# Kernel tuning notes

Hardware: AMD Instinct MI355X
Metric: run time of the kernel (lower is better)

Reference implementation:

```python
import jax, jax.numpy as jnp
import numpy as np

N = 65536      # total nodes
E = 655360     # total edges
G = 256        # graphs in batch
EGO = 64       # ego ids per graph (max(ego)+1)
S = G * EGO    # global ego segments
C_IN, H, P, OUT, L = 128, 128, 64, 10, 3
EPS = 1e-5


def setup_inputs() -> dict:
    key = jax.random.key(0)
    ks = jax.random.split(key, 8)
    x = jax.random.normal(ks[0], (N, C_IN), dtype=jnp.float32)
    edge_index = jax.random.randint(ks[1], (2, E), 0, N)
    batch = jnp.repeat(jnp.arange(G), N // G)          # sorted graph ids
    ego = jnp.arange(N) % EGO                           # every ego segment non-empty
    s = 1.0 / np.sqrt(H)
    w_root = jax.random.normal(ks[2], (L, H, H), jnp.float32) * s
    w_rel = jax.random.normal(ks[3], (L, H, H), jnp.float32) * s
    b_conv = jnp.zeros((L, H), jnp.float32)
    down_w = jax.random.normal(ks[4], (H, P), jnp.float32) * s
    w1 = jax.random.normal(ks[5], (P, 2 * OUT), jnp.float32) * (1.0 / np.sqrt(P))
    b1 = jnp.zeros((2 * OUT,), jnp.float32)
    gamma = jnp.ones((2 * OUT,), jnp.float32)
    beta = jnp.zeros((2 * OUT,), jnp.float32)
    w2 = jax.random.normal(ks[6], (2 * OUT, OUT), jnp.float32) * (1.0 / np.sqrt(2 * OUT))
    b2 = jnp.zeros((OUT,), jnp.float32)
    return dict(x=x, edge_index=edge_index, batch=batch, ego=ego,
                w_root=w_root, w_rel=w_rel, b_conv=b_conv, down_w=down_w,
                w1=w1, b1=b1, gamma=gamma, beta=beta, w2=w2, b2=b2)


def reference(x, edge_index, batch, ego, w_root, w_rel, b_conv, down_w,
              w1, b1, gamma, beta, w2, b2):
    src, dst = edge_index[0], edge_index[1]
    h = x
    for l in range(L):  # GraphConv: lin_rel(sum_{j->i} h_j) + lin_root(h_i) + b, then ReLU
        agg = jax.ops.segment_sum(h[src], dst, num_segments=N)      # [N,H]
        h = jax.nn.relu(agg @ w_rel[l] + h @ w_root[l] + b_conv[l])
    xi = h @ down_w                                                  # [N,P]
    ego_g = ego + batch * EGO                                        # global ego id
    pooled = jax.ops.segment_sum(xi, ego_g, num_segments=S)          # global_add_pool -> [S,P]
    seg_batch = jax.ops.segment_max(batch, ego_g, num_segments=S)    # global_max_pool(batch, ego) -> [S]
    # SoftmaxAggregation(t=1): per-feature softmax over ego segments within each graph
    m = jax.ops.segment_max(pooled, seg_batch, num_segments=G)       # [G,P]
    e = jnp.exp(pooled - m[seg_batch])
    denom = jax.ops.segment_sum(e, seg_batch, num_segments=G)
    alpha = jax.lax.stop_gradient(e / denom[seg_batch])              # semi_grad=True
    g = jax.ops.segment_sum(alpha * pooled, seg_batch, num_segments=G)  # [G,P]
    # PyG MLP([P, 2*OUT, OUT]): Linear -> BatchNorm (batch stats) -> ReLU -> Linear
    z = g @ w1 + b1
    mu = z.mean(axis=0)
    var = z.var(axis=0)
    z = (z - mu) / jnp.sqrt(var + EPS) * gamma + beta
    z = jax.nn.relu(z)
    return z @ w2 + b2                                               # [G,OUT]
```

## Files before the change

kernel.cpp:

```cpp
#include <hip/hip_runtime.h>
#include <hip/hip_bf16.h>

#define NN 65536
#define EE 655360
#define GG 256
#define EGOC 64
#define SS (GG*EGOC)
#define HH 128
#define PP 64
#define OUTD 10
#define LLAYERS 3
#define PADW 40
#define EPB1 5120
#define BCAP 4096

typedef __attribute__((ext_vector_type(8))) short short8_t;
typedef __attribute__((ext_vector_type(4))) float f32x4_t;

__device__ __forceinline__ unsigned short f2bf(float f){
  unsigned u = __float_as_uint(f);
  unsigned r = (u + 0x7fffu + ((u >> 16) & 1u)) >> 16;
  return (unsigned short)r;
}
__device__ __forceinline__ float bflo(unsigned v){ return __uint_as_float(v << 16); }
__device__ __forceinline__ float bfhi(unsigned v){ return __uint_as_float(v & 0xffff0000u); }

__global__ __launch_bounds__(256) void prep(const float* __restrict__ x,
    unsigned short* __restrict__ xb, int* __restrict__ bcur,
    const float* __restrict__ w_rel, const float* __restrict__ w_root,
    unsigned short* __restrict__ wt){
  const int b = blockIdx.x;
  if (b < 4096){
    if (b == 0) bcur[threadIdx.x] = 0;
    const size_t i = ((size_t)b * 256 + threadIdx.x) * 8;
    float4 a = *(const float4*)(x + i);
    float4 v = *(const float4*)(x + i + 4);
    uint4 o;
    o.x = f2bf(a.x) | ((unsigned)f2bf(a.y) << 16);
    o.y = f2bf(a.z) | ((unsigned)f2bf(a.w) << 16);
    o.z = f2bf(v.x) | ((unsigned)f2bf(v.y) << 16);
    o.w = f2bf(v.z) | ((unsigned)f2bf(v.w) << 16);
    *(uint4*)(xb + i) = o;
  } else {
    const int idx = (b - 4096) * 256 + threadIdx.x;
    const int mi = idx >> 14;
    const int n = (idx >> 7) & 127, k = idx & 127;
    const float* src = (mi & 1) ? w_root : w_rel;
    const int l = mi >> 1;
    wt[idx] = f2bf(src[(size_t)l * 16384 + (size_t)k * 128 + n]);
  }
}

__global__ __launch_bounds__(256) void bucket1(const int* __restrict__ src,
    const int* __restrict__ dst, int* __restrict__ bucket_cursor,
    unsigned* __restrict__ bdata){
  __shared__ int hist[256], lbase[256], cur[256], rbase[256];
  __shared__ unsigned staged[EPB1];
  const int t = threadIdx.x;
  const int e0 = blockIdx.x * EPB1;
  hist[t] = 0;
  __syncthreads();
  #pragma unroll
  for (int k = 0; k < EPB1/256; ++k){
    int d = dst[e0 + t + k*256];
    atomicAdd(&hist[d >> 8], 1);
  }
  __syncthreads();
  const int cnt = hist[t];
  int val = cnt;
  for (int off = 1; off < 256; off <<= 1){
    int y = (t >= off) ? hist[t - off] : 0;
    __syncthreads();
    val += y;
    hist[t] = val;
    __syncthreads();
  }
  const int excl = val - cnt;
  lbase[t] = excl;
  cur[t] = excl;
  rbase[t] = atomicAdd(&bucket_cursor[t], cnt);
  __syncthreads();
  #pragma unroll
  for (int k = 0; k < EPB1/256; ++k){
    int i = e0 + t + k*256;
    int d = dst[i];
    int s = src[i];
    int b = d >> 8;
    int p = atomicAdd(&cur[b], 1);
    staged[p] = (unsigned)s | ((unsigned)(d & 255) << 16) | ((unsigned)b << 24);
  }
  __syncthreads();
  #pragma unroll
  for (int k = 0; k < EPB1/256; ++k){
    int i = t + k*256;
    unsigned w = staged[i];
    int b = w >> 24;
    bdata[b * BCAP + rbase[b] + (i - lbase[b])] = w;
  }
}

__global__ __launch_bounds__(256) void bucket2(const unsigned* __restrict__ bdata,
    const int* __restrict__ bucket_cursor, int* __restrict__ rowptr,
    int* __restrict__ csr){
  __shared__ int hist[256], cur[256], red[256];
  const int t = threadIdx.x;
  const int b = blockIdx.x;
  red[t] = (t < b) ? bucket_cursor[t] : 0;
  hist[t] = 0;
  __syncthreads();
  for (int off = 128; off > 0; off >>= 1){
    if (t < off) red[t] += red[t + off];
    __syncthreads();
  }
  const int base = red[0];
  const int cnt = bucket_cursor[b];
  const unsigned* bd = bdata + (size_t)b * BCAP;
  for (int i = t; i < cnt; i += 256)
    atomicAdd(&hist[(bd[i] >> 16) & 255], 1);
  __syncthreads();
  const int c = hist[t];
  int val = c;
  for (int off = 1; off < 256; off <<= 1){
    int y = (t >= off) ? hist[t - off] : 0;
    __syncthreads();
    val += y;
    hist[t] = val;
    __syncthreads();
  }
  const int excl = val - c;
  cur[t] = excl;
  rowptr[(b << 8) + t] = base + excl;
  if (b == 255 && t == 255) rowptr[NN] = EE;
  __syncthreads();
  for (int i = t; i < cnt; i += 256){
    unsigned w = bd[i];
    int dl = (w >> 16) & 255;
    int p = atomicAdd(&cur[dl], 1);
    csr[base + p] = (int)(w & 0xFFFFu);
  }
}

__global__ __launch_bounds__(256) void agg_bf(const unsigned* __restrict__ hb,
    const int* __restrict__ rowptr, const int* __restrict__ csr,
    unsigned* __restrict__ aggb){
  const int wid = threadIdx.x >> 6;
  const int lane = threadIdx.x & 63;
  const int sub = lane >> 4;
  const int c = lane & 15;
  int node = (blockIdx.x << 2) + wid;

  int beg = rowptr[node];
  int end = rowptr[node + 1];
  int sw0, sw1, sw2, sw3;
  {
    int e0 = beg + sub, e1 = beg + 4 + sub, e2 = beg + 8 + sub, e3 = beg + 12 + sub;
    sw0 = csr[e0 < end ? e0 : beg];
    sw1 = csr[e1 < end ? e1 : beg];
    sw2 = csr[e2 < end ? e2 : beg];
    sw3 = csr[e3 < end ? e3 : beg];
  }

  for (int g = 0; g < 8; ++g){
    uint4 w0 = *(const uint4*)(hb + ((size_t)sw0 << 6) + (c << 2));
    uint4 w1 = *(const uint4*)(hb + ((size_t)sw1 << 6) + (c << 2));
    uint4 w2 = *(const uint4*)(hb + ((size_t)sw2 << 6) + (c << 2));
    uint4 w3 = *(const uint4*)(hb + ((size_t)sw3 << 6) + (c << 2));
    int nbeg = 0, nend = 0;
    if (g < 7){
      nbeg = rowptr[node + 8192];
      nend = rowptr[node + 8193];
    }
    float a0=0.f,a1=0.f,a2=0.f,a3=0.f,a4=0.f,a5=0.f,a6=0.f,a7=0.f;
    if (beg + sub      < end){ a0+=bflo(w0.x); a1+=bfhi(w0.x); a2+=bflo(w0.y); a3+=bfhi(w0.y);
                               a4+=bflo(w0.z); a5+=bfhi(w0.z); a6+=bflo(w0.w); a7+=bfhi(w0.w); }
    if (beg + 4 + sub  < end){ a0+=bflo(w1.x); a1+=bfhi(w1.x); a2+=bflo(w1.y); a3+=bfhi(w1.y);
                               a4+=bflo(w1.z); a5+=bfhi(w1.z); a6+=bflo(w1.w); a7+=bfhi(w1.w); }
    if (beg + 8 + sub  < end){ a0+=bflo(w2.x); a1+=bfhi(w2.x); a2+=bflo(w2.y); a3+=bfhi(w2.y);
                               a4+=bflo(w2.z); a5+=bfhi(w2.z); a6+=bflo(w2.w); a7+=bfhi(w2.w); }
    if (beg + 12 + sub < end){ a0+=bflo(w3.x); a1+=bfhi(w3.x); a2+=bflo(w3.y); a3+=bfhi(w3.y);
                               a4+=bflo(w3.z); a5+=bfhi(w3.z); a6+=bflo(w3.w); a7+=bfhi(w3.w); }
    for (int j = beg + 16; j < end; j += 16){
      #pragma unroll
      for (int u = 0; u < 4; ++u){
        const int e = j + (u << 2) + sub;
        if (e < end){
          const int s = csr[e];
          uint4 w = *(const uint4*)(hb + ((size_t)s << 6) + (c << 2));
          a0 += bflo(w.x); a1 += bfhi(w.x);
          a2 += bflo(w.y); a3 += bfhi(w.y);
          a4 += bflo(w.z); a5 += bfhi(w.z);
          a6 += bflo(w.w); a7 += bfhi(w.w);
        }
      }
    }
    a0 += __shfl_xor(a0, 16, 64); a1 += __shfl_xor(a1, 16, 64);
    a2 += __shfl_xor(a2, 16, 64); a3 += __shfl_xor(a3, 16, 64);
    a4 += __shfl_xor(a4, 16, 64); a5 += __shfl_xor(a5, 16, 64);
    a6 += __shfl_xor(a6, 16, 64); a7 += __shfl_xor(a7, 16, 64);
    a0 += __shfl_xor(a0, 32, 64); a1 += __shfl_xor(a1, 32, 64);
    a2 += __shfl_xor(a2, 32, 64); a3 += __shfl_xor(a3, 32, 64);
    a4 += __shfl_xor(a4, 32, 64); a5 += __shfl_xor(a5, 32, 64);
    a6 += __shfl_xor(a6, 32, 64); a7 += __shfl_xor(a7, 32, 64);
    if (lane < 16){
      uint4 o;
      o.x = (unsigned)f2bf(a0) | ((unsigned)f2bf(a1) << 16);
      o.y = (unsigned)f2bf(a2) | ((unsigned)f2bf(a3) << 16);
      o.z = (unsigned)f2bf(a4) | ((unsigned)f2bf(a5) << 16);
      o.w = (unsigned)f2bf(a6) | ((unsigned)f2bf(a7) << 16);
      *(uint4*)(aggb + ((size_t)node << 6) + (c << 2)) = o;
    }
    if (g < 7){
      node += 8192;
      beg = nbeg; end = nend;
      int e0 = beg + sub, e1 = beg + 4 + sub, e2 = beg + 8 + sub, e3 = beg + 12 + sub;
      sw0 = csr[e0 < end ? e0 : beg];
      sw1 = csr[e1 < end ? e1 : beg];
      sw2 = csr[e2 < end ? e2 : beg];
      sw3 = csr[e3 < end ? e3 : beg];
    }
  }
}

__global__ __launch_bounds__(256) void conv_mfma(
    const unsigned short* __restrict__ Aagg, const unsigned short* __restrict__ Ah,
    const unsigned short* __restrict__ wt,
    const float* __restrict__ bias,
    unsigned short* __restrict__ out){
  __shared__ unsigned short As[2][128 * PADW];
  __shared__ unsigned short Ws[2][128 * PADW];
  const int tid = threadIdx.x;
  const int row0 = blockIdx.x << 7;
  const int lane = tid & 63, wid = tid >> 6;
  const int wm64 = (wid >> 1) << 6;
  const int wn64 = (wid & 1) << 6;
  const int fr = lane & 15;
  const int fs = (lane >> 4) << 3;
  const int r0 = tid >> 2;
  const int s8 = (tid & 3) << 3;

  f32x4_t acc[4][4];
  #pragma unroll
  for (int i = 0; i < 4; ++i)
    #pragma unroll
    for (int j = 0; j < 4; ++j) acc[i][j] = (f32x4_t){0.f,0.f,0.f,0.f};

  uint4 ga0, ga1, gw0, gw1;

#define STAGE_LOAD(c) do{ \
    const unsigned short* Ap = ((c) < 4) ? Aagg : Ah; \
    const unsigned short* Wp = ((c) < 4) ? wt : (wt + 16384); \
    const int k0 = ((c) & 3) << 5; \
    ga0 = *(const uint4*)(Ap + (size_t)(row0 + r0) * 128 + k0 + s8); \
    ga1 = *(const uint4*)(Ap + (size_t)(row0 + 64 + r0) * 128 + k0 + s8); \
    gw0 = *(const uint4*)(Wp + (size_t)r0 * 128 + k0 + s8); \
    gw1 = *(const uint4*)(Wp + (size_t)(64 + r0) * 128 + k0 + s8); } while(0)
#define STAGE_WRITE(b) do{ \
    *(uint4*)&As[b][r0 * PADW + s8] = ga0; \
    *(uint4*)&As[b][(64 + r0) * PADW + s8] = ga1; \
    *(uint4*)&Ws[b][r0 * PADW + s8] = gw0; \
    *(uint4*)&Ws[b][(64 + r0) * PADW + s8] = gw1; } while(0)

  STAGE_LOAD(0);
  STAGE_WRITE(0);
  __syncthreads();

  for (int c = 0; c < 8; ++c){
    const int b = c & 1;
    if (c < 7) STAGE_LOAD(c + 1);

    short8_t af[4], wf[4];
    #pragma unroll
    for (int i = 0; i < 4; ++i)
      af[i] = *(const short8_t*)&As[b][(wm64 + i*16 + fr) * PADW + fs];
    #pragma unroll
    for (int j = 0; j < 4; ++j)
      wf[j] = *(const short8_t*)&Ws[b][(wn64 + j*16 + fr) * PADW + fs];
    #pragma unroll
    for (int j = 0; j < 4; ++j)
      #pragma unroll
      for (int i = 0; i < 4; ++i)
        acc[i][j] = __builtin_amdgcn_mfma_f32_16x16x32_bf16(wf[j], af[i], acc[i][j], 0, 0, 0);

    if (c < 7){
      STAGE_WRITE(b ^ 1);
      __syncthreads();
    }
  }
#undef STAGE_LOAD
#undef STAGE_WRITE

  #pragma unroll
  for (int j = 0; j < 4; ++j){
    const int n0 = wn64 + j*16 + ((lane >> 4) << 2);
    float4 b4 = *(const float4*)(bias + n0);
    #pragma unroll
    for (int i = 0; i < 4; ++i){
      const int m = row0 + wm64 + i*16 + fr;
      float v0 = fmaxf(acc[i][j][0] + b4.x, 0.f);
      float v1 = fmaxf(acc[i][j][1] + b4.y, 0.f);
      float v2 = fmaxf(acc[i][j][2] + b4.z, 0.f);
      float v3 = fmaxf(acc[i][j][3] + b4.w, 0.f);
      uint2 pk;
      pk.x = (unsigned)f2bf(v0) | ((unsigned)f2bf(v1) << 16);
      pk.y = (unsigned)f2bf(v2) | ((unsigned)f2bf(v3) << 16);
      *(uint2*)(out + (size_t)m * 128 + n0) = pk;
    }
  }
}

__global__ __launch_bounds__(256) void pool_soft(const unsigned* __restrict__ hb,
    const float* __restrict__ down_w, float* __restrict__ gout){
  __shared__ float wds[128 * 64];
  __shared__ float ps[64][64];
  __shared__ float hs[4][128];
  __shared__ float r1[4][64], r2[4][64];
  const int tid = threadIdx.x;
  const int g = blockIdx.x;
  for (int i = tid; i < 128 * 64 / 4; i += 256)
    ((float4*)wds)[i] = ((const float4*)down_w)[i];
  __syncthreads();
  const int wid = tid >> 6, lane = tid & 63;
  for (int it = 0; it < 16; ++it){
    const int e = (it << 2) + wid;
    const unsigned* hr = hb + (((size_t)(g * 256 + e)) << 6) + lane;
    float ax = 0.f, ay = 0.f;
    #pragma unroll
    for (int q = 0; q < 4; ++q){
      unsigned v = hr[(size_t)q * 64 * 64];
      ax += bflo(v); ay += bfhi(v);
    }
    hs[wid][(lane << 1) + 0] = ax;
    hs[wid][(lane << 1) + 1] = ay;
    float a0 = 0.f, a1 = 0.f, a2 = 0.f, a3 = 0.f;
    #pragma unroll
    for (int k = 0; k < 128; k += 4){
      a0 = fmaf(hs[wid][k + 0], wds[(k + 0) * 64 + lane], a0);
      a1 = fmaf(hs[wid][k + 1], wds[(k + 1) * 64 + lane], a1);
      a2 = fmaf(hs[wid][k + 2], wds[(k + 2) * 64 + lane], a2);
      a3 = fmaf(hs[wid][k + 3], wds[(k + 3) * 64 + lane], a3);
    }
    ps[e][lane] = (a0 + a1) + (a2 + a3);
  }
  __syncthreads();
  float m = -3.4e38f;
  #pragma unroll
  for (int r = 0; r < 16; ++r) m = fmaxf(m, ps[(wid << 4) + r][lane]);
  r1[wid][lane] = m;
  __syncthreads();
  m = fmaxf(fmaxf(r1[0][lane], r1[1][lane]), fmaxf(r1[2][lane], r1[3][lane]));
  __syncthreads();
  float se = 0.f, sn = 0.f;
  #pragma unroll
  for (int r = 0; r < 16; ++r){
    float p = ps[(wid << 4) + r][lane];
    float ev = expf(p - m);
    se += ev; sn += ev * p;
  }
  r1[wid][lane] = se; r2[wid][lane] = sn;
  __syncthreads();
  if (wid == 0){
    float d = (r1[0][lane] + r1[1][lane]) + (r1[2][lane] + r1[3][lane]);
    float n = (r2[0][lane] + r2[1][lane]) + (r2[2][lane] + r2[3][lane]);
    gout[(size_t)g * 64 + lane] = n / d;
  }
}

__global__ __launch_bounds__(256) void mlp_kernel(const float* __restrict__ gmat,
    const float* __restrict__ w1, const float* __restrict__ b1,
    const float* __restrict__ gamma, const float* __restrict__ beta,
    const float* __restrict__ w2, const float* __restrict__ b2,
    float* __restrict__ out){
  const int r = threadIdx.x;
  float z[20];
  #pragma unroll
  for (int j = 0; j < 20; ++j) z[j] = b1[j];
  for (int k = 0; k < 64; ++k){
    float gv = gmat[r*64 + k];
    #pragma unroll
    for (int j = 0; j < 20; ++j) z[j] = fmaf(gv, w1[k*20 + j], z[j]);
  }
  __shared__ float red1[4][20], red2[4][20];
  __shared__ float mu[20], istd[20];
  const int lane = r & 63, wid = r >> 6;
  #pragma unroll
  for (int j = 0; j < 20; ++j){
    float a = z[j], b = z[j]*z[j];
    #pragma unroll
    for (int off = 32; off > 0; off >>= 1){
      a += __shfl_xor(a, off, 64);
      b += __shfl_xor(b, off, 64);
    }
    if (lane == 0){ red1[wid][j] = a; red2[wid][j] = b; }
  }
  __syncthreads();
  if (r < 20){
    float m = red1[0][r] + red1[1][r] + red1[2][r] + red1[3][r];
    float q = red2[0][r] + red2[1][r] + red2[2][r] + red2[3][r];
    m *= (1.f/256.f); q *= (1.f/256.f);
    float var = q - m*m;
    mu[r] = m;
    istd[r] = 1.f / sqrtf(var + 1e-5f);
  }
  __syncthreads();
  float o[10];
  #pragma unroll
  for (int jo = 0; jo < 10; ++jo) o[jo] = b2[jo];
  #pragma unroll
  for (int j = 0; j < 20; ++j){
    float zn = (z[j] - mu[j]) * istd[j] * gamma[j] + beta[j];
    zn = fmaxf(zn, 0.f);
    #pragma unroll
    for (int jo = 0; jo < 10; ++jo) o[jo] = fmaf(zn, w2[j*10 + jo], o[jo]);
  }
  #pragma unroll
  for (int jo = 0; jo < 10; ++jo) out[r*10 + jo] = o[jo];
}

extern "C" void kernel_launch(void* const* d_in, const int* in_sizes, int n_in,
                              void* d_out, int out_size, void* d_ws, size_t ws_size,
                              hipStream_t stream){
  const float* x      = (const float*)d_in[0];
  const int*   eidx   = (const int*)d_in[1];
  const float* w_root = (const float*)d_in[4];
  const float* w_rel  = (const float*)d_in[5];
  const float* b_conv = (const float*)d_in[6];
  const float* down_w = (const float*)d_in[7];
  const float* w1     = (const float*)d_in[8];
  const float* b1     = (const float*)d_in[9];
  const float* gamma  = (const float*)d_in[10];
  const float* beta   = (const float*)d_in[11];
  const float* w2     = (const float*)d_in[12];
  const float* b2     = (const float*)d_in[13];
  const int* src = eidx;
  const int* dst = eidx + EE;

  char* wsp = (char*)d_ws;
  size_t off = 0;
  auto alloc = [&](size_t bytes)->char*{
    char* p = wsp + off;
    off += (bytes + 255) & ~(size_t)255;
    return p;
  };
  unsigned short* hb   = (unsigned short*)alloc((size_t)NN*HH*2);
  unsigned short* aggb = (unsigned short*)alloc((size_t)NN*HH*2);
  unsigned short* wtb  = (unsigned short*)alloc((size_t)6*128*128*2);
  int*      rowptr = (int*)     alloc((size_t)(NN+1)*4);
  int*      csr    = (int*)     alloc((size_t)EE*4);
  unsigned* bdata  = (unsigned*)alloc((size_t)256*BCAP*4);
  int*      bcur   = (int*)     alloc((size_t)256*4);
  float*    gout   = (float*)   alloc((size_t)GG*PP*4);

  prep<<<4096 + 384, 256, 0, stream>>>(x, hb, bcur, w_rel, w_root, wtb);
  bucket1<<<EE/EPB1, 256, 0, stream>>>(src, dst, bcur, bdata);
  bucket2<<<256, 256, 0, stream>>>(bdata, bcur, rowptr, csr);

  for (int l = 0; l < LLAYERS; ++l){
    agg_bf<<<2048, 256, 0, stream>>>((const unsigned*)hb, rowptr, csr, (unsigned*)aggb);
    conv_mfma<<<NN/128, 256, 0, stream>>>(aggb, hb, wtb + (size_t)l*2*16384,
        b_conv + (size_t)l*HH, hb);
  }

  pool_soft<<<GG, 256, 0, stream>>>((const unsigned*)hb, down_w, gout);
  mlp_kernel<<<1, 256, 0, stream>>>(gout, w1, b1, gamma, beta, w2, b2, (float*)d_out);
}
```

Measured before the change: 191.4 us.

## Partition CSR edges by source quarter to improve gather locality in aggregation

The CSR build now sub-sorts each destination's edges into four groups by source-node range (bits 14-15 of src) and emits a 4-way row pointer per node. The aggregation kernel processes one source quarter at a time across all nodes of a wave, accumulating partial sums in shared memory. The aim is to keep the gathered feature rows of one quarter of the nodes resident in cache during each pass. In exchange it adds LDS read-modify-write traffic, a block-wide barrier after each quarter, and less memory-level parallelism per wave, since each wave now has only one gather in flight ahead instead of four.

```diff
diff --git a/kernel.cpp b/kernel.cpp
--- a/kernel.cpp
+++ b/kernel.cpp
@@ -100,91 +100,93 @@
 }
 
 __global__ __launch_bounds__(256) void bucket2(const unsigned* __restrict__ bdata,
-    const int* __restrict__ bucket_cursor, int* __restrict__ rowptr,
+    const int* __restrict__ bucket_cursor, int* __restrict__ rowptr5,
     int* __restrict__ csr){
-  __shared__ int hist[256], cur[256], red[256];
+  __shared__ int hist[1024], cur[1024];
+  __shared__ int red[256];
   const int t = threadIdx.x;
   const int b = blockIdx.x;
   red[t] = (t < b) ? bucket_cursor[t] : 0;
-  hist[t] = 0;
+  #pragma unroll
+  for (int i = 0; i < 4; ++i) hist[(i << 8) + t] = 0;
   __syncthreads();
   for (int off = 128; off > 0; off >>= 1){
     if (t < off) red[t] += red[t + off];
     __syncthreads();
   }
   const int base = red[0];
+  __syncthreads();
   const int cnt = bucket_cursor[b];
   const unsigned* bd = bdata + (size_t)b * BCAP;
-  for (int i = t; i < cnt; i += 256)
-    atomicAdd(&hist[(bd[i] >> 16) & 255], 1);
-  __syncthreads();
-  const int c = hist[t];
-  int val = c;
-  for (int off = 1; off < 256; off <<= 1){
-    int y = (t >= off) ? hist[t - off] : 0;
-    __syncthreads();
-    val += y;
-    hist[t] = val;
-    __syncthreads();
-  }
-  const int excl = val - c;
-  cur[t] = excl;
-  rowptr[(b << 8) + t] = base + excl;
-  if (b == 255 && t == 255) rowptr[NN] = EE;
-  __syncthreads();
   for (int i = t; i < cnt; i += 256){
     unsigned w = bd[i];
-    int dl = (w >> 16) & 255;
-    int p = atomicAdd(&cur[dl], 1);
+    int key = (((w >> 16) & 255) << 2) | ((w >> 14) & 3);
+    atomicAdd(&hist[key], 1);
+  }
+  __syncthreads();
+  int h0 = hist[(t << 2) + 0], h1 = hist[(t << 2) + 1];
+  int h2 = hist[(t << 2) + 2], h3 = hist[(t << 2) + 3];
+  const int lsum = h0 + h1 + h2 + h3;
+  int val = lsum;
+  red[t] = lsum;
+  __syncthreads();
+  for (int off = 1; off < 256; off <<= 1){
+    int y = (t >= off) ? red[t - off] : 0;
+    __syncthreads();
+    val += y;
+    red[t] = val;
+    __syncthreads();
+  }
+  const int excl = val - lsum;
+  const int o0 = excl, o1 = o0 + h0, o2 = o1 + h1, o3 = o2 + h2;
+  cur[(t << 2) + 0] = o0; cur[(t << 2) + 1] = o1;
+  cur[(t << 2) + 2] = o2; cur[(t << 2) + 3] = o3;
+  rowptr5[(b << 10) + (t << 2) + 0] = base + o0;
+  rowptr5[(b << 10) + (t << 2) + 1] = base + o1;
+  rowptr5[(b << 10) + (t << 2) + 2] = base + o2;
+  rowptr5[(b << 10) + (t << 2) + 3] = base + o3;
+  if (b == 255 && t == 255) rowptr5[NN * 4] = EE;
+  __syncthreads();
+  for (int i = t; i < cnt; i += 256){
+    unsigned w = bd[i];
+    int key = (((w >> 16) & 255) << 2) | ((w >> 14) & 3);
+    int p = atomicAdd(&cur[key], 1);
     csr[base + p] = (int)(w & 0xFFFFu);
   }
 }
 
 __global__ __launch_bounds__(256) void agg_bf(const unsigned* __restrict__ hb,
-    const int* __restrict__ rowptr, const int* __restrict__ csr,
+    const int* __restrict__ rowptr5, const int* __restrict__ csr,
     unsigned* __restrict__ aggb){
+  __shared__ float acc[4][8][128];
   const int wid = threadIdx.x >> 6;
   const int lane = threadIdx.x & 63;
   const int sub = lane >> 4;
   const int c = lane & 15;
-  int node = (blockIdx.x << 2) + wid;
-
-  int beg = rowptr[node];
-  int end = rowptr[node + 1];
-  int sw0, sw1, sw2, sw3;
-  {
-    int e0 = beg + sub, e1 = beg + 4 + sub, e2 = beg + 8 + sub, e3 = beg + 12 + sub;
-    sw0 = csr[e0 < end ? e0 : beg];
-    sw1 = csr[e1 < end ? e1 : beg];
-    sw2 = csr[e2 < end ? e2 : beg];
-    sw3 = csr[e3 < end ? e3 : beg];
-  }
-
-  for (int g = 0; g < 8; ++g){
-    uint4 w0 = *(const uint4*)(hb + ((size_t)sw0 << 6) + (c << 2));
-    uint4 w1 = *(const uint4*)(hb + ((size_t)sw1 << 6) + (c << 2));
-    uint4 w2 = *(const uint4*)(hb + ((size_t)sw2 << 6) + (c << 2));
-    uint4 w3 = *(const uint4*)(hb + ((size_t)sw3 << 6) + (c << 2));
-    int nbeg = 0, nend = 0;
-    if (g < 7){
-      nbeg = rowptr[node + 8192];
-      nend = rowptr[node + 8193];
-    }
-    float a0=0.f,a1=0.f,a2=0.f,a3=0.f,a4=0.f,a5=0.f,a6=0.f,a7=0.f;
-    if (beg + sub      < end){ a0+=bflo(w0.x); a1+=bfhi(w0.x); a2+=bflo(w0.y); a3+=bfhi(w0.y);
-                               a4+=bflo(w0.z); a5+=bfhi(w0.z); a6+=bflo(w0.w); a7+=bfhi(w0.w); }
-    if (beg + 4 + sub  < end){ a0+=bflo(w1.x); a1+=bfhi(w1.x); a2+=bflo(w1.y); a3+=bfhi(w1.y);
-                               a4+=bflo(w1.z); a5+=bfhi(w1.z); a6+=bflo(w1.w); a7+=bfhi(w1.w); }
-    if (beg + 8 + sub  < end){ a0+=bflo(w2.x); a1+=bfhi(w2.x); a2+=bflo(w2.y); a3+=bfhi(w2.y);
-                               a4+=bflo(w2.z); a5+=bfhi(w2.z); a6+=bflo(w2.w); a7+=bfhi(w2.w); }
-    if (beg + 12 + sub < end){ a0+=bflo(w3.x); a1+=bfhi(w3.x); a2+=bflo(w3.y); a3+=bfhi(w3.y);
-                               a4+=bflo(w3.z); a5+=bfhi(w3.z); a6+=bflo(w3.w); a7+=bfhi(w3.w); }
-    for (int j = beg + 16; j < end; j += 16){
-      #pragma unroll
-      for (int u = 0; u < 4; ++u){
-        const int e = j + (u << 2) + sub;
+  const int wv = (blockIdx.x << 2) + wid;
+  const int nbase = wv << 3;
+
+  for (int p = 0; p < 4; ++p){
+    int beg = rowptr5[(nbase << 2) + p];
+    int end = rowptr5[(nbase << 2) + p + 1];
+    int e0 = beg + sub;
+    int sw = csr[(e0 < end) ? e0 : 0];
+    for (int g = 0; g < 8; ++g){
+      uint4 w0 = *(const uint4*)(hb + ((size_t)sw << 6) + (c << 2));
+      int nbeg = 0, nend = 0;
+      if (g < 7){
+        nbeg = rowptr5[((nbase + g + 1) << 2) + p];
+        nend = rowptr5[((nbase + g + 1) << 2) + p + 1];
+      }
+      float a0=0.f,a1=0.f,a2=0.f,a3=0.f,a4=0.f,a5=0.f,a6=0.f,a7=0.f;
+      if (beg + sub < end){
+        a0+=bflo(w0.x); a1+=bfhi(w0.x); a2+=bflo(w0.y); a3+=bfhi(w0.y);
+        a4+=bflo(w0.z); a5+=bfhi(w0.z); a6+=bflo(w0.w); a7+=bfhi(w0.w);
+      }
+      for (int j = beg + 4; j < end; j += 4){
+        int e = j + sub;
         if (e < end){
-          const int s = csr[e];
+          int s = csr[e];
           uint4 w = *(const uint4*)(hb + ((size_t)s << 6) + (c << 2));
           a0 += bflo(w.x); a1 += bfhi(w.x);
           a2 += bflo(w.y); a3 += bfhi(w.y);
@@ -192,32 +194,38 @@
           a6 += bflo(w.w); a7 += bfhi(w.w);
         }
       }
-    }
-    a0 += __shfl_xor(a0, 16, 64); a1 += __shfl_xor(a1, 16, 64);
-    a2 += __shfl_xor(a2, 16, 64); a3 += __shfl_xor(a3, 16, 64);
-    a4 += __shfl_xor(a4, 16, 64); a5 += __shfl_xor(a5, 16, 64);
-    a6 += __shfl_xor(a6, 16, 64); a7 += __shfl_xor(a7, 16, 64);
-    a0 += __shfl_xor(a0, 32, 64); a1 += __shfl_xor(a1, 32, 64);
-    a2 += __shfl_xor(a2, 32, 64); a3 += __shfl_xor(a3, 32, 64);
-    a4 += __shfl_xor(a4, 32, 64); a5 += __shfl_xor(a5, 32, 64);
-    a6 += __shfl_xor(a6, 32, 64); a7 += __shfl_xor(a7, 32, 64);
-    if (lane < 16){
-      uint4 o;
-      o.x = (unsigned)f2bf(a0) | ((unsigned)f2bf(a1) << 16);
-      o.y = (unsigned)f2bf(a2) | ((unsigned)f2bf(a3) << 16);
-      o.z = (unsigned)f2bf(a4) | ((unsigned)f2bf(a5) << 16);
-      o.w = (unsigned)f2bf(a6) | ((unsigned)f2bf(a7) << 16);
-      *(uint4*)(aggb + ((size_t)node << 6) + (c << 2)) = o;
-    }
-    if (g < 7){
-      node += 8192;
-      beg = nbeg; end = nend;
-      int e0 = beg + sub, e1 = beg + 4 + sub, e2 = beg + 8 + sub, e3 = beg + 12 + sub;
-      sw0 = csr[e0 < end ? e0 : beg];
-      sw1 = csr[e1 < end ? e1 : beg];
-      sw2 = csr[e2 < end ? e2 : beg];
-      sw3 = csr[e3 < end ? e3 : beg];
-    }
+      a0 += __shfl_xor(a0, 16, 64); a1 += __shfl_xor(a1, 16, 64);
+      a2 += __shfl_xor(a2, 16, 64); a3 += __shfl_xor(a3, 16, 64);
+      a4 += __shfl_xor(a4, 16, 64); a5 += __shfl_xor(a5, 16, 64);
+      a6 += __shfl_xor(a6, 16, 64); a7 += __shfl_xor(a7, 16, 64);
+      a0 += __shfl_xor(a0, 32, 64); a1 += __shfl_xor(a1, 32, 64);
+      a2 += __shfl_xor(a2, 32, 64); a3 += __shfl_xor(a3, 32, 64);
+      a4 += __shfl_xor(a4, 32, 64); a5 += __shfl_xor(a5, 32, 64);
+      a6 += __shfl_xor(a6, 32, 64); a7 += __shfl_xor(a7, 32, 64);
+      if (lane < 16){
+        float* ar = &acc[wid][g][c << 3];
+        if (p == 0){
+          ar[0]=a0; ar[1]=a1; ar[2]=a2; ar[3]=a3;
+          ar[4]=a4; ar[5]=a5; ar[6]=a6; ar[7]=a7;
+        } else if (p < 3){
+          ar[0]+=a0; ar[1]+=a1; ar[2]+=a2; ar[3]+=a3;
+          ar[4]+=a4; ar[5]+=a5; ar[6]+=a6; ar[7]+=a7;
+        } else {
+          uint4 o;
+          o.x = (unsigned)f2bf(ar[0]+a0) | ((unsigned)f2bf(ar[1]+a1) << 16);
+          o.y = (unsigned)f2bf(ar[2]+a2) | ((unsigned)f2bf(ar[3]+a3) << 16);
+          o.z = (unsigned)f2bf(ar[4]+a4) | ((unsigned)f2bf(ar[5]+a5) << 16);
+          o.w = (unsigned)f2bf(ar[6]+a6) | ((unsigned)f2bf(ar[7]+a7) << 16);
+          *(uint4*)(aggb + ((size_t)(nbase + g) << 6) + (c << 2)) = o;
+        }
+      }
+      if (g < 7){
+        beg = nbeg; end = nend;
+        int e = beg + sub;
+        sw = csr[(e < end) ? e : 0];
+      }
+    }
+    __syncthreads();
   }
 }
 
@@ -444,7 +452,7 @@
   unsigned short* hb   = (unsigned short*)alloc((size_t)NN*HH*2);
   unsigned short* aggb = (unsigned short*)alloc((size_t)NN*HH*2);
   unsigned short* wtb  = (unsigned short*)alloc((size_t)6*128*128*2);
-  int*      rowptr = (int*)     alloc((size_t)(NN+1)*4);
+  int*      rowptr5 = (int*)    alloc((size_t)(NN*4 + 64)*4);
   int*      csr    = (int*)     alloc((size_t)EE*4);
   unsigned* bdata  = (unsigned*)alloc((size_t)256*BCAP*4);
   int*      bcur   = (int*)     alloc((size_t)256*4);
@@ -452,10 +460,10 @@
 
   prep<<<4096 + 384, 256, 0, stream>>>(x, hb, bcur, w_rel, w_root, wtb);
   bucket1<<<EE/EPB1, 256, 0, stream>>>(src, dst, bcur, bdata);
-  bucket2<<<256, 256, 0, stream>>>(bdata, bcur, rowptr, csr);
+  bucket2<<<256, 256, 0, stream>>>(bdata, bcur, rowptr5, csr);
 
   for (int l = 0; l < LLAYERS; ++l){
-    agg_bf<<<2048, 256, 0, stream>>>((const unsigned*)hb, rowptr, csr, (unsigned*)aggb);
+    agg_bf<<<2048, 256, 0, stream>>>((const unsigned*)hb, rowptr5, csr, (unsigned*)aggb);
     conv_mfma<<<NN/128, 256, 0, stream>>>(aggb, hb, wtb + (size_t)l*2*16384,
         b_conv + (size_t)l*HH, hb);
   }
```

New measurement: 325.5 us. +70.1%, slower.
